# Optimization experiments

Hardware: AMD Instinct MI355X
Metric: run time of the kernel (lower is better)

## Reference

```python
import jax, jax.numpy as jnp
import numpy as np

WINDOW, SIM_TH, GAMMA, L_MAX, NUM_HEADS = 32, 0.7, 0.8, 1024, 8


def setup_inputs() -> dict:
    key = jax.random.key(0)
    ks = jax.random.split(key, 12)
    B, N, F, D, S, V, C = 8, 16384, 1024, 512, 64, 30522, 4
    padded_bags = jax.random.normal(ks[0], (B, N, F), jnp.float32)
    lengths = jax.random.randint(ks[1], (B,), N // 4, N + 1)
    key_padding_mask = jnp.arange(N)[None, :] >= lengths[:, None]  # True = pad (tail)
    input_ids = jax.random.randint(ks[2], (B, S), 0, V)
    attention_mask = jnp.ones((B, S), jnp.int32)

    def xav(k, shape):
        lim = np.sqrt(6.0 / (shape[0] + shape[1]))
        return jax.random.uniform(k, shape, jnp.float32, -lim, lim)

    emb_table = jax.random.normal(ks[3], (V, 768), jnp.float32) * 0.02
    return dict(
        padded_bags=padded_bags, key_padding_mask=key_padding_mask,
        input_ids=input_ids, attention_mask=attention_mask,
        emb_table=emb_table,
        W_tp=xav(ks[4], (768, D)), b_tp=jnp.zeros((D,), jnp.float32),
        W_enc=xav(ks[5], (F, D)), b_enc=jnp.zeros((D,), jnp.float32),
        ln_g=jnp.ones((D,), jnp.float32), ln_b=jnp.zeros((D,), jnp.float32),
        Wq=xav(ks[6], (D, D)), bq=jnp.zeros((D,), jnp.float32),
        Wk=xav(ks[7], (D, D)), bk=jnp.zeros((D,), jnp.float32),
        Wv=xav(ks[8], (D, D)), bv=jnp.zeros((D,), jnp.float32),
        Wo=xav(ks[9], (D, D)), bo=jnp.zeros((D,), jnp.float32),
        W_cls=xav(ks[10], (D, C)), b_cls=jnp.zeros((C,), jnp.float32),
    )


def reference(padded_bags, key_padding_mask, input_ids, attention_mask,
              emb_table, W_tp, b_tp, W_enc, b_enc, ln_g, ln_b,
              Wq, bq, Wk, bk, Wv, bv, Wo, bo, W_cls, b_cls):
    B, N, _ = padded_bags.shape
    D = W_enc.shape[1]
    # --- frozen text encoder surrogate (DistilBERT is frozen + no_grad in original):
    # token embedding + masked mean pooling stands in for the CLS feature [B,768]
    tok = emb_table[input_ids]                                   # [B,S,768]
    am = attention_mask[..., None].astype(jnp.float32)
    text_feat = (tok * am).sum(1) / jnp.maximum(am.sum(1), 1.0)
    text_feat = jax.lax.stop_gradient(text_feat)
    text_emb = text_feat @ W_tp + b_tp                           # [B,D]
    # --- feature encoder: Linear + LayerNorm + ReLU (dropout = eval identity) ---
    h = padded_bags @ W_enc + b_enc                              # [B,N,D]
    mu = h.mean(-1, keepdims=True)
    var = ((h - mu) ** 2).mean(-1, keepdims=True)
    img = jax.nn.relu(ln_g * (h - mu) / jnp.sqrt(var + 1e-5) + ln_b)
    valid = ~key_padding_mask                                    # [B,N]
    # --- Stage 1: sliding-window (size 32) cosine-similarity redundancy pruning ---
    fn = img / (jnp.linalg.norm(img, axis=-1, keepdims=True) + 1e-8)
    neg = jnp.full((B, N), -jnp.inf, jnp.float32)
    max_sim = neg
    for w in range(1, WINDOW + 1):                               # fixed small window loop
        sim_w = (fn[:, w:] * fn[:, :-w]).sum(-1)                 # [B,N-w]
        sim_w = jnp.where(valid[:, :-w], sim_w, -jnp.inf)
        max_sim = jnp.maximum(max_sim, jnp.concatenate([neg[:, :w], sim_w], axis=1))
    keep1 = valid & (max_sim < SIM_TH)                           # [B,N]
    # --- Stage 2: language-guided top-k by text relevance, kept in original order ---
    rel = jnp.einsum('bnd,bd->bn', img, text_emb)
    rel_m = jnp.where(keep1, rel, -jnp.inf)
    n_kept = keep1.sum(-1)
    k_b = jnp.clip((GAMMA * n_kept.astype(jnp.float32)).astype(jnp.int32), 1, L_MAX)
    _, idx = jax.lax.top_k(rel_m, L_MAX)                         # [B,L_MAX]
    sel = jnp.arange(L_MAX)[None, :] < k_b[:, None]
    idx_sorted = jnp.sort(jnp.where(sel, idx, N), axis=-1)       # sort -> original order
    mask2 = idx_sorted < N
    feat2 = jnp.take_along_axis(img, jnp.clip(idx_sorted, 0, N - 1)[..., None], axis=1)
    feat2 = jnp.where(mask2[..., None], feat2, 0.0)              # [B,L_MAX,D] zero-repadded
    # --- Stage 3: sequential visual token compression (adjacent-pair mean pooling) ---
    M = L_MAX // 2
    f2 = feat2.reshape(B, M, 2, D)
    pm = mask2.reshape(B, M, 2).astype(jnp.float32)
    feat3 = (f2 * pm[..., None]).sum(2) / jnp.maximum(pm.sum(2), 1.0)[..., None]  # [B,M,D]
    # --- cross-modal MHA aggregator (text query; zero-padded keys DO attend, as in original) ---
    H = NUM_HEADS
    dh = D // H
    q = (text_emb @ Wq + bq).reshape(B, H, dh)
    k = (feat3 @ Wk + bk).reshape(B, M, H, dh)
    v = (feat3 @ Wv + bv).reshape(B, M, H, dh)
    scores = jnp.einsum('bhd,bmhd->bhm', q, k) / np.float32(np.sqrt(dh))
    attn = jax.nn.softmax(scores, axis=-1)
    ctx = jnp.einsum('bhm,bmhd->bhd', attn, v).reshape(B, D)
    out = ctx @ Wo + bo
    return out @ W_cls + b_cls                                   # [B,num_classes]
```

## Files before the change

kernel.cpp:

```cpp
#include <hip/hip_runtime.h>
#include <hip/hip_bf16.h>
#include <math.h>
#include <stdint.h>

#define B_    8
#define N_    16384
#define F_    1024
#define D_    512
#define S_    64
#define H_    8
#define DH_   64
#define LMAX_ 1024
#define M2_   512
#define WIN_  32
#define NTOK_ (B_ * N_)

typedef __attribute__((ext_vector_type(8)))  short bf16x8;
typedef __attribute__((ext_vector_type(16))) float f32x16;

#define S_OF(r) (((r) >> 1) & 3)

static __device__ __forceinline__ float wred_sum(float v) {
    #pragma unroll
    for (int d = 1; d < 64; d <<= 1) v += __shfl_xor(v, d, 64);
    return v;
}

static __device__ __forceinline__ void bf8_to_f32(uint4 q, float* a) {
    a[0] = __uint_as_float(q.x << 16); a[1] = __uint_as_float(q.x & 0xffff0000u);
    a[2] = __uint_as_float(q.y << 16); a[3] = __uint_as_float(q.y & 0xffff0000u);
    a[4] = __uint_as_float(q.z << 16); a[5] = __uint_as_float(q.z & 0xffff0000u);
    a[6] = __uint_as_float(q.w << 16); a[7] = __uint_as_float(q.w & 0xffff0000u);
}

static __device__ __forceinline__ unsigned short bf16r(float x) {
    unsigned int b = __float_as_uint(x);
    return (unsigned short)((b + 0x7FFFu + ((b >> 16) & 1u)) >> 16);
}

static __device__ __forceinline__ void split_bf(float x, unsigned short& h, unsigned short& l) {
    unsigned int b = __float_as_uint(x);
    unsigned int hb = (b + 0x7FFFu + ((b >> 16) & 1u)) >> 16;
    h = (unsigned short)hb;
    float r = x - __uint_as_float(hb << 16);
    l = bf16r(r);
}

static __device__ __forceinline__ void split8(float4 f0, float4 f1, bf16x8& hi, bf16x8& lo) {
    float xs[8] = { f0.x, f0.y, f0.z, f0.w, f1.x, f1.y, f1.z, f1.w };
    unsigned int hp[4], lp[4];
    #pragma unroll
    for (int i = 0; i < 4; i++) {
        unsigned int b0 = __float_as_uint(xs[2*i]), b1 = __float_as_uint(xs[2*i+1]);
        hp[i] = (b0 >> 16) | (b1 & 0xffff0000u);
        float r0 = xs[2*i]   - __uint_as_float(b0 & 0xffff0000u);
        float r1 = xs[2*i+1] - __uint_as_float(b1 & 0xffff0000u);
        lp[i] = (__float_as_uint(r0) >> 16) | (__float_as_uint(r1) & 0xffff0000u);
    }
    union { uint4 u; bf16x8 v; } a, c;
    a.u = make_uint4(hp[0], hp[1], hp[2], hp[3]);
    c.u = make_uint4(lp[0], lp[1], lp[2], lp[3]);
    hi = a.v; lo = c.v;
}

static __device__ __forceinline__ void gll16(const void* g, void* l) {
    __builtin_amdgcn_global_load_lds(
        (const __attribute__((address_space(1))) unsigned int*)g,
        (__attribute__((address_space(3))) unsigned int*)l, 16, 0, 0);
}

__global__ void k_detect(const unsigned char* mb, int nbytes, int* flag) {
    int found = 0;
    for (int i = blockIdx.x * blockDim.x + threadIdx.x; i < nbytes; i += gridDim.x * blockDim.x)
        if ((i & 3) && mb[i]) found = 1;
    if (found) atomicOr(flag, 1);
}

__global__ void k_valid(const void* maskp, const int* flag, unsigned char* v) {
    int i = blockIdx.x * 256 + threadIdx.x;
    if (i >= NTOK_) return;
    int pad;
    if (*flag) pad = (((const unsigned char*)maskp)[i] != 0);
    else       pad = (((const int*)maskp)[i] != 0);
    v[i] = pad ? 0 : 1;
}

__global__ void k_text_feat(const float* emb, const int* ids, const int* am, float* tf) {
    int b = blockIdx.x;
    __shared__ int   sid[S_];
    __shared__ float sam[S_];
    int t = threadIdx.x;
    if (t < S_) { sid[t] = ids[b * S_ + t]; sam[t] = (float)am[b * S_ + t]; }
    __syncthreads();
    float asum = 0.f;
    for (int s = 0; s < S_; s++) asum += sam[s];
    float denom = fmaxf(asum, 1.0f);
    for (int d = t; d < 768; d += blockDim.x) {
        float acc = 0.f;
        for (int s = 0; s < S_; s++) acc += emb[(long)sid[s] * 768 + d] * sam[s];
        tf[b * 768 + d] = acc / denom;
    }
}

__global__ void k_rowmm(const float* in, const float* W, const float* bias,
                        float* out, int E, int Nn) {
    int b = blockIdx.x, d = threadIdx.x;
    __shared__ float sin[768];
    for (int e = d; e < E; e += blockDim.x) sin[e] = in[b * E + e];
    __syncthreads();
    float acc = bias[d];
    for (int e = 0; e < E; e++) acc = fmaf(sin[e], W[(long)e * Nn + d], acc);
    out[b * Nn + d] = acc;
}

__global__ __launch_bounds__(256) void k_bsplit_sw(const float* __restrict__ W,
                                                   unsigned short* __restrict__ bh,
                                                   unsigned short* __restrict__ bl) {
    __shared__ float tile[32][33];
    int e0 = blockIdx.x * 32;
    int d0 = blockIdx.y * 32;
    int t = threadIdx.x;
    int r = t >> 3, c4 = (t & 7) * 4;
    float4 v = *(const float4*)(W + (long)(e0 + r) * D_ + d0 + c4);
    tile[r][c4] = v.x; tile[r][c4 + 1] = v.y; tile[r][c4 + 2] = v.z; tile[r][c4 + 3] = v.w;
    __syncthreads();
    if (t < 128) {
        int c = t & 31, kq = t >> 5;
        int col = d0 + c;
        float xs[8];
        #pragma unroll
        for (int i = 0; i < 8; i++) xs[i] = tile[kq * 8 + i][c];
        unsigned short h[8], l[8];
        #pragma unroll
        for (int i = 0; i < 8; i++) split_bf(xs[i], h[i], l[i]);
        uint4 ph, pl;
        ph.x = h[0] | ((unsigned)h[1] << 16); ph.y = h[2] | ((unsigned)h[3] << 16);
        ph.z = h[4] | ((unsigned)h[5] << 16); ph.w = h[6] | ((unsigned)h[7] << 16);
        pl.x = l[0] | ((unsigned)l[1] << 16); pl.y = l[2] | ((unsigned)l[3] << 16);
        pl.z = l[4] | ((unsigned)l[5] << 16); pl.w = l[6] | ((unsigned)l[7] << 16);
        int Q = (e0 >> 3) + kq;
        int Qo = (Q & ~3) | ((Q & 3) ^ S_OF(col & 7));
        *(uint4*)(bh + (long)col * 1024 + Qo * 8) = ph;
        *(uint4*)(bl + (long)col * 1024 + Qo * 8) = pl;
    }
}

__global__ __launch_bounds__(256) void k_gemm3(const float* __restrict__ A,
                                               const unsigned short* __restrict__ Bh2,
                                               const unsigned short* __restrict__ Bl2,
                                               const float* __restrict__ bias,
                                               float* __restrict__ C) {
    __shared__ __align__(16) float ldsA[128][32];
    __shared__ __align__(16) unsigned short ldsB[2][128][32];
    int bid = blockIdx.x;
    int wg = (bid & 7) * 512 + (bid >> 3);
    int bn = wg & 3, bm = wg >> 2;
    int tid = threadIdx.x;
    int w = tid >> 6, lane = tid & 63;
    int r32 = lane & 31, kg = lane >> 5;
    int wr = w >> 1, wc = w & 1;
    int s8 = r32 & 7;

    const float* agbase = nullptr;
    const unsigned short* bgbase = nullptr;
    if (w < 2) {
        int rl = lane >> 3, qs = lane & 7;
        agbase = A + (long)(bm * 128 + w * 64 + rl) * 1024 + ((qs ^ rl) * 4);
    } else {
        const unsigned short* plane = (w == 2) ? Bh2 : Bl2;
        int lrow = lane >> 2, lq = lane & 3;
        bgbase = plane + (long)(bn * 128 + lrow) * 1024 + lq * 8;
    }

    f32x16 acc[2][2];
    #pragma unroll
    for (int i = 0; i < 2; i++)
        #pragma unroll
        for (int j = 0; j < 2; j++)
            #pragma unroll
            for (int r = 0; r < 16; r++) acc[i][j][r] = 0.f;

    for (int kt = 0; kt < 1024; kt += 32) {
        if (w < 2) {
            #pragma unroll
            for (int j = 0; j < 8; j++)
                gll16(agbase + (long)j * 8 * 1024 + kt, &ldsA[w * 64 + j * 8][0]);
        } else {
            #pragma unroll
            for (int j = 0; j < 8; j++)
                gll16(bgbase + (long)j * 16 * 1024 + kt, &ldsB[w - 2][j * 16][0]);
        }
        __syncthreads();
        #pragma unroll
        for (int k2 = 0; k2 < 2; k2++) {
            int qA = k2 * 4 + kg * 2;
            int qs0 = (qA ^ s8) * 4;
            int qs1 = ((qA + 1) ^ s8) * 4;
            bf16x8 a_h[2], a_l[2];
            #pragma unroll
            for (int rf = 0; rf < 2; rf++) {
                int ar = wr * 64 + rf * 32 + r32;
                float4 f0 = *(const float4*)&ldsA[ar][qs0];
                float4 f1 = *(const float4*)&ldsA[ar][qs1];
                split8(f0, f1, a_h[rf], a_l[rf]);
            }
            int qb = k2 * 2 + kg;
            bf16x8 b_h[2], b_l[2];
            #pragma unroll
            for (int cf = 0; cf < 2; cf++) {
                int bc = wc * 64 + cf * 32 + r32;
                int q = (qb ^ S_OF(r32)) * 8;
                b_h[cf] = *(const bf16x8*)&ldsB[0][bc][q];
                b_l[cf] = *(const bf16x8*)&ldsB[1][bc][q];
            }
            #pragma unroll
            for (int rf = 0; rf < 2; rf++)
                #pragma unroll
                for (int cf = 0; cf < 2; cf++) {
                    acc[rf][cf] = __builtin_amdgcn_mfma_f32_32x32x16_bf16(a_h[rf], b_h[cf], acc[rf][cf], 0, 0, 0);
                    acc[rf][cf] = __builtin_amdgcn_mfma_f32_32x32x16_bf16(a_h[rf], b_l[cf], acc[rf][cf], 0, 0, 0);
                    acc[rf][cf] = __builtin_amdgcn_mfma_f32_32x32x16_bf16(a_l[rf], b_h[cf], acc[rf][cf], 0, 0, 0);
                }
        }
        __syncthreads();
    }
    #pragma unroll
    for (int rf = 0; rf < 2; rf++)
        #pragma unroll
        for (int cf = 0; cf < 2; cf++) {
            int col = bn * 128 + wc * 64 + cf * 32 + r32;
            float bv = bias[col];
            #pragma unroll
            for (int r = 0; r < 16; r++) {
                int row = bm * 128 + wr * 64 + rf * 32 + (r & 3) + 8 * (r >> 2) + 4 * kg;
                C[(long)row * D_ + col] = acc[rf][cf][r] + bv;
            }
        }
}

#define GPAD 40
__global__ __launch_bounds__(256, 3) void k_gemm_mfma(const float* __restrict__ A,
                                                      const unsigned short* __restrict__ Bth,
                                                      const unsigned short* __restrict__ Btl,
                                                      const float* __restrict__ bias,
                                                      float* __restrict__ C) {
    __shared__ __align__(16) unsigned short As[2][64][GPAD];
    __shared__ __align__(16) unsigned short Bs[2][256][GPAD];
    int bm = blockIdx.x, bn = blockIdx.y;
    int tid = threadIdx.x;
    int w = tid >> 6, lane = tid & 63;
    int r32 = lane & 31, kg = lane >> 5;
    f32x16 acc[2][2];
    #pragma unroll
    for (int i = 0; i < 2; i++)
        #pragma unroll
        for (int j = 0; j < 2; j++)
            #pragma unroll
            for (int r = 0; r < 16; r++) acc[i][j][r] = 0.f;
    int arow = tid >> 2, aq = tid & 3;
    const float* abase = A + (long)(bm * 64 + arow) * 1024 + aq * 8;
    const unsigned short* bhbase = Bth + (long)(bn * 256 + tid) * 1024;
    const unsigned short* blbase = Btl + (long)(bn * 256 + tid) * 1024;
    float4 pa0 = *(const float4*)abase;
    float4 pa1 = *(const float4*)(abase + 4);
    for (int kt = 0; kt < 1024; kt += 32) {
        {
            float xs[8] = { pa0.x, pa0.y, pa0.z, pa0.w, pa1.x, pa1.y, pa1.z, pa1.w };
            unsigned short h[8], l[8];
            #pragma unroll
            for (int i = 0; i < 8; i++) split_bf(xs[i], h[i], l[i]);
            uint4 ph, pl;
            ph.x = h[0] | ((unsigned)h[1] << 16); ph.y = h[2] | ((unsigned)h[3] << 16);
            ph.z = h[4] | ((unsigned)h[5] << 16); ph.w = h[6] | ((unsigned)h[7] << 16);
            pl.x = l[0] | ((unsigned)l[1] << 16); pl.y = l[2] | ((unsigned)l[3] << 16);
            pl.z = l[4] | ((unsigned)l[5] << 16); pl.w = l[6] | ((unsigned)l[7] << 16);
            *(uint4*)&As[0][arow][aq * 8] = ph;
            *(uint4*)&As[1][arow][aq * 8] = pl;
        }
        {
            const uint4* ph = (const uint4*)(bhbase + kt);
            const uint4* pl = (const uint4*)(blbase + kt);
            #pragma unroll
            for (int q = 0; q < 4; q++) {
                *(uint4*)&Bs[0][tid][q * 8] = ph[q];
                *(uint4*)&Bs[1][tid][q * 8] = pl[q];
            }
        }
        __syncthreads();
        if (kt + 32 < 1024) {
            const float* ap = abase + kt + 32;
            pa0 = *(const float4*)ap;
            pa1 = *(const float4*)(ap + 4);
        }
        #pragma unroll
        for (int k2 = 0; k2 < 2; k2++) {
            int ko = k2 * 16 + kg * 8;
            bf16x8 ah[2], al[2], bh[2], blv[2];
            #pragma unroll
            for (int rf = 0; rf < 2; rf++) {
                ah[rf] = *(const bf16x8*)&As[0][rf * 32 + r32][ko];
                al[rf] = *(const bf16x8*)&As[1][rf * 32 + r32][ko];
            }
            #pragma unroll
            for (int cf = 0; cf < 2; cf++) {
                bh[cf]  = *(const bf16x8*)&Bs[0][w * 64 + cf * 32 + r32][ko];
                blv[cf] = *(const bf16x8*)&Bs[1][w * 64 + cf * 32 + r32][ko];
            }
            #pragma unroll
            for (int rf = 0; rf < 2; rf++)
                #pragma unroll
                for (int cf = 0; cf < 2; cf++) {
                    acc[rf][cf] = __builtin_amdgcn_mfma_f32_32x32x16_bf16(ah[rf], bh[cf],  acc[rf][cf], 0, 0, 0);
                    acc[rf][cf] = __builtin_amdgcn_mfma_f32_32x32x16_bf16(ah[rf], blv[cf], acc[rf][cf], 0, 0, 0);
                    acc[rf][cf] = __builtin_amdgcn_mfma_f32_32x32x16_bf16(al[rf], bh[cf],  acc[rf][cf], 0, 0, 0);
                }
        }
        __syncthreads();
    }
    #pragma unroll
    for (int rf = 0; rf < 2; rf++)
        #pragma unroll
        for (int cf = 0; cf < 2; cf++) {
            int col = bn * 256 + w * 64 + cf * 32 + r32;
            float bv = bias[col];
            #pragma unroll
            for (int r = 0; r < 16; r++) {
                int row = bm * 64 + rf * 32 + (r & 3) + 8 * (r >> 2) + 4 * kg;
                C[(long)row * D_ + col] = acc[rf][cf][r] + bv;
            }
        }
}

__global__ __launch_bounds__(256) void k_bsplit(const float* __restrict__ W,
                                                unsigned short* __restrict__ bh,
                                                unsigned short* __restrict__ bl) {
    __shared__ float tile[32][33];
    int e0 = blockIdx.x * 32;
    int d0 = blockIdx.y * 32;
    int t = threadIdx.x;
    int r = t >> 3;
    int c = (t & 7) * 4;
    float4 v = *(const float4*)(W + (long)(e0 + r) * D_ + d0 + c);
    tile[r][c] = v.x; tile[r][c + 1] = v.y; tile[r][c + 2] = v.z; tile[r][c + 3] = v.w;
    __syncthreads();
    ushort4 h4, l4;
    unsigned short hh, ll;
    float x0 = tile[c + 0][r], x1 = tile[c + 1][r], x2 = tile[c + 2][r], x3 = tile[c + 3][r];
    split_bf(x0, hh, ll); h4.x = hh; l4.x = ll;
    split_bf(x1, hh, ll); h4.y = hh; l4.y = ll;
    split_bf(x2, hh, ll); h4.z = hh; l4.z = ll;
    split_bf(x3, hh, ll); h4.w = hh; l4.w = ll;
    *(ushort4*)(bh + (long)(d0 + r) * 1024 + e0 + c) = h4;
    *(ushort4*)(bl + (long)(d0 + r) * 1024 + e0 + c) = l4;
}

__global__ __launch_bounds__(256) void k_ln(float* h, const float* g, const float* bb,
                                            const float* temb, float* rnorm, float* rel,
                                            unsigned short* fnb, float2* stats, int write_img) {
    int wid = threadIdx.x >> 6, lane = threadIdx.x & 63;
    long row = (long)blockIdx.x * 4 + wid;
    int b = (int)(row >> 14);
    float* hp = h + row * (long)D_;
    int c0 = lane * 4, c1 = 256 + lane * 4;
    float4 x0 = *(float4*)(hp + c0);
    float4 x1 = *(float4*)(hp + c1);
    float x[8] = { x0.x, x0.y, x0.z, x0.w, x1.x, x1.y, x1.z, x1.w };
    float s = 0.f;
    #pragma unroll
    for (int i = 0; i < 8; i++) s += x[i];
    s = wred_sum(s);
    float mu = s * (1.0f / 512.0f);
    float var = 0.f;
    #pragma unroll
    for (int i = 0; i < 8; i++) { float d = x[i] - mu; var += d * d; }
    var = wred_sum(var) * (1.0f / 512.0f);
    float inv = 1.0f / sqrtf(var + 1e-5f);
    float4 g0 = *(const float4*)(g + c0), g1 = *(const float4*)(g + c1);
    float4 b0 = *(const float4*)(bb + c0), b1 = *(const float4*)(bb + c1);
    float gg[8] = { g0.x, g0.y, g0.z, g0.w, g1.x, g1.y, g1.z, g1.w };
    float bbv[8] = { b0.x, b0.y, b0.z, b0.w, b1.x, b1.y, b1.z, b1.w };
    float y[8], sq = 0.f;
    #pragma unroll
    for (int i = 0; i < 8; i++) {
        y[i] = fmaxf(gg[i] * (x[i] - mu) * inv + bbv[i], 0.0f);
        sq += y[i] * y[i];
    }
    if (write_img) {
        float4 o0 = { y[0], y[1], y[2], y[3] }, o1 = { y[4], y[5], y[6], y[7] };
        *(float4*)(hp + c0) = o0;
        *(float4*)(hp + c1) = o1;
    }
    sq = wred_sum(sq);
    float rn = 1.0f / (sqrtf(sq) + 1e-8f);
    if (fnb) {
        ushort4 u0, u1;
        u0.x = bf16r(y[0] * rn); u0.y = bf16r(y[1] * rn);
        u0.z = bf16r(y[2] * rn); u0.w = bf16r(y[3] * rn);
        u1.x = bf16r(y[4] * rn); u1.y = bf16r(y[5] * rn);
        u1.z = bf16r(y[6] * rn); u1.w = bf16r(y[7] * rn);
        *(ushort4*)(fnb + row * D_ + c0) = u0;
        *(ushort4*)(fnb + row * D_ + c1) = u1;
    }
    const float* tp = temb + (long)b * D_;
    float4 t0 = *(const float4*)(tp + c0), t1 = *(const float4*)(tp + c1);
    float tt[8] = { t0.x, t0.y, t0.z, t0.w, t1.x, t1.y, t1.z, t1.w };
    float rl = 0.f;
    #pragma unroll
    for (int i = 0; i < 8; i++) rl = fmaf(y[i], tt[i], rl);
    rl = wred_sum(rl);
    if (lane == 0) { rnorm[row] = rn; rel[row] = rl; stats[row] = make_float2(mu, inv); }
}

__global__ __launch_bounds__(256) void k_simg(const unsigned short* __restrict__ fnb,
                                              const unsigned char* __restrict__ vld,
                                              int* __restrict__ keep) {
    int wid = threadIdx.x >> 6, lane = threadIdx.x & 63;
    int T = (blockIdx.x * 4 + wid) * 32;
    int r32 = lane & 31, kg = lane >> 5;
    int prevok = (T & (N_ - 1)) != 0;
    const unsigned short* arow  = fnb + (long)(T + r32) * D_ + kg * 8;
    const unsigned short* b0row = fnb + (long)((prevok ? T - 32 : T) + r32) * D_ + kg * 8;

    f32x16 g0, g1;
    #pragma unroll
    for (int r = 0; r < 16; r++) { g0[r] = 0.f; g1[r] = 0.f; }
    #pragma unroll 4
    for (int kt = 0; kt < D_; kt += 16) {
        bf16x8 a  = *(const bf16x8*)(arow + kt);
        bf16x8 b0 = *(const bf16x8*)(b0row + kt);
        g0 = __builtin_amdgcn_mfma_f32_32x32x16_bf16(a, b0, g0, 0, 0, 0);
        g1 = __builtin_amdgcn_mfma_f32_32x32x16_bf16(a, a,  g1, 0, 0, 0);
    }
    int okc0 = prevok ? (int)vld[T - 32 + r32] : 0;
    int okc1 = (int)vld[T + r32];
    float ms[16];
    #pragma unroll
    for (int r = 0; r < 16; r++) {
        int i = (r & 3) + 8 * (r >> 2) + 4 * kg;
        float v = -INFINITY;
        if (okc0 && r32 >= i) v = g0[r];
        if (okc1 && r32 < i)  v = fmaxf(v, g1[r]);
        #pragma unroll
        for (int d = 1; d < 32; d <<= 1) v = fmaxf(v, __shfl_xor(v, d, 64));
        ms[r] = v;
    }
    if (r32 == 0) {
        #pragma unroll
        for (int r = 0; r < 16; r++) {
            int i = (r & 3) + 8 * (r >> 2) + 4 * kg;
            int t = T + i;
            keep[t] = (vld[t] && ms[r] < 0.7f) ? 1 : 0;
        }
    }
}

#define CHUNK 28
#define KROWS 60
__global__ __launch_bounds__(256) void k_sim(const float* img, const float* rnorm,
                                             const unsigned char* vld, int* keep) {
    __shared__ __hip_bfloat16 fnbs[KROWS][D_];
    long c0 = (long)blockIdx.x * CHUNK;
    int tid = threadIdx.x;
    for (int idx = tid; idx < KROWS * (D_ / 8); idx += 256) {
        int rr = idx / (D_ / 8);
        int cc = (idx % (D_ / 8)) * 8;
        long grow = c0 - WIN_ + rr;
        if (grow < 0) grow = 0;
        if (grow >= NTOK_) grow = NTOK_ - 1;
        float rn = rnorm[grow];
        const float* p = img + grow * (long)D_ + cc;
        float4 u = *(const float4*)p, w = *(const float4*)(p + 4);
        fnbs[rr][cc + 0] = __float2bfloat16(u.x * rn);
        fnbs[rr][cc + 1] = __float2bfloat16(u.y * rn);
        fnbs[rr][cc + 2] = __float2bfloat16(u.z * rn);
        fnbs[rr][cc + 3] = __float2bfloat16(u.w * rn);
        fnbs[rr][cc + 4] = __float2bfloat16(w.x * rn);
        fnbs[rr][cc + 5] = __float2bfloat16(w.y * rn);
        fnbs[rr][cc + 6] = __float2bfloat16(w.z * rn);
        fnbs[rr][cc + 7] = __float2bfloat16(w.w * rn);
    }
    __syncthreads();
    int wid = tid >> 6, lane = tid & 63;
    for (int ti = 0; ti < 7; ti++) {
        int tloc = wid * 7 + ti;
        long t = c0 + tloc;
        if (t >= NTOK_) continue;
        int lr = WIN_ + tloc;
        int tl = (int)(t & (N_ - 1));
        float a[8];
        bf8_to_f32(*(const uint4*)&fnbs[lr][lane * 8], a);
        int wmax = tl < WIN_ ? tl : WIN_;
        float msim = -INFINITY;
        for (int w = 1; w <= wmax; w++) {
            if (!vld[t - w]) continue;
            float bvv[8];
            bf8_to_f32(*(const uint4*)&fnbs[lr - w][lane * 8], bvv);
            float p = 0.f;
            #pragma unroll
            for (int i = 0; i < 8; i++) p = fmaf(a[i], bvv[i], p);
            p = wred_sum(p);
            msim = fmaxf(msim, p);
        }
        int kp = (vld[t] && (msim < 0.7f)) ? 1 : 0;
        if (lane == 0) keep[t] = kp;
    }
}

static __device__ void scan1024(int* tot, int tid) {
    if (tid < 64) {
        int vals[16], s = 0;
        #pragma unroll
        for (int i = 0; i < 16; i++) vals[i] = tot[tid * 16 + i];
        #pragma unroll
        for (int i = 0; i < 16; i++) { int t = vals[i]; vals[i] = s; s += t; }
        int inc = s;
        #pragma unroll
        for (int d = 1; d < 64; d <<= 1) {
            int v = __shfl_up(inc, d, 64);
            if ((tid & 63) >= d) inc += v;
        }
        int excl = inc - s;
        #pragma unroll
        for (int i = 0; i < 16; i++) tot[tid * 16 + i] = vals[i] + excl;
    }
}

__global__ __launch_bounds__(1024) void k_topk(const float* rel, const int* keep, int* idxo) {
    int b = blockIdx.x, tid = threadIdx.x;
    const float* relb = rel + (long)b * N_;
    const int* keepb  = keep + (long)b * N_;
    __shared__ unsigned int hist[256];
    __shared__ int toti[1024];
    __shared__ unsigned int s_prefix;
    __shared__ int s_rem, s_k;

    unsigned int key[16];
    int base = tid * 16, nk_local = 0;
    #pragma unroll
    for (int j = 0; j < 16; j++) {
        int i = base + j;
        float r = relb[i];
        int kp = keepb[i];
        unsigned int bits = __float_as_uint(r);
        unsigned int kk = (bits & 0x80000000u) ? ~bits : (bits | 0x80000000u);
        key[j] = kp ? kk : 0u;
        nk_local += kp;
    }
    toti[tid] = nk_local; __syncthreads();
    for (int o = 512; o > 0; o >>= 1) { if (tid < o) toti[tid] += toti[tid + o]; __syncthreads(); }
    if (tid == 0) {
        int n_kept = toti[0];
        int k = (int)(0.8f * (float)n_kept);
        if (k < 1) k = 1; if (k > LMAX_) k = LMAX_;
        s_k = k; s_rem = k; s_prefix = 0u;
    }
    __syncthreads();

    for (int pass = 0; pass < 4; pass++) {
        int shift = 24 - pass * 8;
        unsigned int himask = (pass == 0) ? 0u : (0xFFFFFFFFu << (shift + 8));
        if (tid < 256) hist[tid] = 0u;
        __syncthreads();
        unsigned int pfx = s_prefix;
        #pragma unroll
        for (int j = 0; j < 16; j++) {
            unsigned int kk = key[j];
            if ((kk & himask) == (pfx & himask))
                atomicAdd(&hist[(kk >> shift) & 255], 1u);
        }
        __syncthreads();
        if (tid == 0) {
            int rem = s_rem;
            unsigned int cum = 0;
            for (int d = 255; d >= 0; d--) {
                unsigned int h = hist[d];
                if (cum + h >= (unsigned int)rem) {
                    s_rem = rem - (int)cum;
                    s_prefix = pfx | ((unsigned int)d << shift);
                    break;
                }
                cum += h;
            }
        }
        __syncthreads();
    }
    unsigned int T = s_prefix;
    int tie_need = s_rem, k = s_k;

    int eq[16], gt[16], eqpre[16];
    int locEq = 0;
    #pragma unroll
    for (int j = 0; j < 16; j++) {
        eq[j] = (key[j] == T); gt[j] = (key[j] > T);
        eqpre[j] = locEq; locEq += eq[j];
    }
    toti[tid] = locEq; __syncthreads();
    scan1024(toti, tid); __syncthreads();
    int eqoff = toti[tid];

    int sel[16], spre[16];
    int locS = 0;
    #pragma unroll
    for (int j = 0; j < 16; j++) {
        int rank = eqoff + eqpre[j];
        sel[j] = gt[j] || (eq[j] && rank < tie_need);
        spre[j] = locS; locS += sel[j];
    }
    __syncthreads();
    toti[tid] = locS; __syncthreads();
    scan1024(toti, tid); __syncthreads();
    int soff = toti[tid];
    #pragma unroll
    for (int j = 0; j < 16; j++)
        if (sel[j]) idxo[b * LMAX_ + soff + spre[j]] = base + j;
    for (int p = k + tid; p < LMAX_; p += 1024) idxo[b * LMAX_ + p] = N_;
}

__global__ void k_feat3(const float* img, const float2* stats, const float* lng,
                        const float* lnb, const int* idxo, float* f3, int recompute) {
    int bm = blockIdx.x;
    int b = bm >> 9, m = bm & 511;
    int i0 = idxo[b * LMAX_ + 2 * m], i1 = idxo[b * LMAX_ + 2 * m + 1];
    int c0 = i0 < N_, c1 = i1 < N_;
    float dn = 1.0f / fmaxf((float)(c0 + c1), 1.0f);
    long r0 = (long)b * N_ + (c0 ? i0 : 0);
    long r1 = (long)b * N_ + (c1 ? i1 : 0);
    int d = threadIdx.x * 4;
    float4 v0 = c0 ? *(const float4*)(img + r0 * D_ + d) : make_float4(0.f, 0.f, 0.f, 0.f);
    float4 v1 = c1 ? *(const float4*)(img + r1 * D_ + d) : make_float4(0.f, 0.f, 0.f, 0.f);
    if (recompute) {
        float4 g4 = *(const float4*)(lng + d);
        float4 b4 = *(const float4*)(lnb + d);
        if (c0) {
            float2 st = stats[r0];
            v0.x = fmaxf(g4.x * (v0.x - st.x) * st.y + b4.x, 0.0f);
            v0.y = fmaxf(g4.y * (v0.y - st.x) * st.y + b4.y, 0.0f);
            v0.z = fmaxf(g4.z * (v0.z - st.x) * st.y + b4.z, 0.0f);
            v0.w = fmaxf(g4.w * (v0.w - st.x) * st.y + b4.w, 0.0f);
        }
        if (c1) {
            float2 st = stats[r1];
            v1.x = fmaxf(g4.x * (v1.x - st.x) * st.y + b4.x, 0.0f);
            v1.y = fmaxf(g4.y * (v1.y - st.x) * st.y + b4.y, 0.0f);
            v1.z = fmaxf(g4.z * (v1.z - st.x) * st.y + b4.z, 0.0f);
            v1.w = fmaxf(g4.w * (v1.w - st.x) * st.y + b4.w, 0.0f);
        }
    }
    float4 o;
    o.x = (v0.x + v1.x) * dn; o.y = (v0.y + v1.y) * dn;
    o.z = (v0.z + v1.z) * dn; o.w = (v0.w + v1.w) * dn;
    *(float4*)(f3 + (long)bm * D_ + d) = o;
}

#define BM 128
#define BN 64
#define BK 32
#define ASTR 136
__global__ __launch_bounds__(256) void k_gemmkv(const float* __restrict__ A,
                                                const float* __restrict__ Wk2, const float* __restrict__ bk2, float* __restrict__ Ck,
                                                const float* __restrict__ Wv2, const float* __restrict__ bv2, float* __restrict__ Cv) {
    __shared__ float As[BK][ASTR];
    __shared__ float Bsf[BK][BN];
    int bm = blockIdx.x;
    int which = blockIdx.y >> 3;
    int bn = blockIdx.y & 7;
    const float* Bw  = which ? Wv2 : Wk2;
    const float* bias = which ? bv2 : bk2;
    float* C = which ? Cv : Ck;
    int tid = threadIdx.x;
    int trow = tid >> 4, tcol = tid & 15;
    float acc[8][4] = {};
    const float* Ab = A + (long)bm * BM * D_;
    const float* Bb = Bw + bn * BN;
    for (int kt = 0; kt < D_; kt += BK) {
        #pragma unroll
        for (int i = 0; i < 4; i++) {
            int f = tid + 256 * i;
            int row = f >> 3, c4 = (f & 7) << 2;
            float4 v = *(const float4*)(Ab + (long)row * D_ + kt + c4);
            As[c4 + 0][row] = v.x; As[c4 + 1][row] = v.y;
            As[c4 + 2][row] = v.z; As[c4 + 3][row] = v.w;
        }
        #pragma unroll
        for (int i = 0; i < 2; i++) {
            int f = tid + 256 * i;
            int row = f >> 4, c4 = (f & 15) << 2;
            *(float4*)&Bsf[row][c4] = *(const float4*)(Bb + (long)(kt + row) * D_ + c4);
        }
        __syncthreads();
        #pragma unroll 8
        for (int kk = 0; kk < BK; kk++) {
            float a[8], bv4[4];
            #pragma unroll
            for (int i = 0; i < 8; i++) a[i] = As[kk][trow * 8 + i];
            #pragma unroll
            for (int j = 0; j < 4; j++) bv4[j] = Bsf[kk][tcol * 4 + j];
            #pragma unroll
            for (int i = 0; i < 8; i++)
                #pragma unroll
                for (int j = 0; j < 4; j++)
                    acc[i][j] = fmaf(a[i], bv4[j], acc[i][j]);
        }
        __syncthreads();
    }
    int c = bn * BN + tcol * 4;
    #pragma unroll
    for (int i = 0; i < 8; i++) {
        long r = (long)bm * BM + trow * 8 + i;
        float4 v;
        v.x = acc[i][0] + bias[c + 0]; v.y = acc[i][1] + bias[c + 1];
        v.z = acc[i][2] + bias[c + 2]; v.w = acc[i][3] + bias[c + 3];
        *(float4*)(C + r * D_ + c) = v;
    }
}

__global__ __launch_bounds__(512) void k_attn(const float* qv, const float* kk,
                                              const float* vv, float* ctx) {
    int bh = blockIdx.x;
    int b = bh >> 3, h = bh & 7;
    __shared__ float qs[DH_];
    __shared__ float sc[M2_];
    __shared__ float red[M2_];
    __shared__ float part[8][DH_];
    int m = threadIdx.x;
    if (m < DH_) qs[m] = qv[b * D_ + h * DH_ + m];
    __syncthreads();
    const float* kp = kk + (long)b * M2_ * D_ + h * DH_;
    float acc = 0.f;
    #pragma unroll
    for (int d = 0; d < DH_; d += 4) {
        float4 kv = *(const float4*)(kp + (long)m * D_ + d);
        acc += qs[d] * kv.x + qs[d + 1] * kv.y + qs[d + 2] * kv.z + qs[d + 3] * kv.w;
    }
    acc *= 0.125f;
    red[m] = acc; __syncthreads();
    for (int o = 256; o > 0; o >>= 1) { if (m < o) red[m] = fmaxf(red[m], red[m + o]); __syncthreads(); }
    float mx = red[0]; __syncthreads();
    float e = expf(acc - mx);
    sc[m] = e; red[m] = e; __syncthreads();
    for (int o = 256; o > 0; o >>= 1) { if (m < o) red[m] += red[m + o]; __syncthreads(); }
    float inv = 1.0f / red[0];
    int g = m >> 6, d = m & 63;
    const float* vp = vv + (long)b * M2_ * D_ + h * DH_ + d;
    float a2 = 0.f;
    #pragma unroll 4
    for (int mm = g * 64; mm < g * 64 + 64; mm++)
        a2 = fmaf(sc[mm], vp[(long)mm * D_], a2);
    part[g][d] = a2; __syncthreads();
    if (m < DH_) {
        float s = 0.f;
        #pragma unroll
        for (int g2 = 0; g2 < 8; g2++) s += part[g2][m];
        ctx[b * D_ + h * DH_ + m] = s * inv;
    }
}

__global__ __launch_bounds__(512) void k_head(const float* ctx, const float* Wo, const float* bo,
                                              const float* Wc, const float* bc,
                                              float* out) {
    int b = blockIdx.x, d = threadIdx.x;
    __shared__ float cl[D_], ol[D_];
    cl[d] = ctx[b * D_ + d]; __syncthreads();
    float acc = bo[d];
    for (int e = 0; e < D_; e++) acc = fmaf(cl[e], Wo[(long)e * D_ + d], acc);
    ol[d] = acc; __syncthreads();
    if (d < 4) {
        float a2 = bc[d];
        for (int e = 0; e < D_; e++) a2 = fmaf(ol[e], Wc[e * 4 + d], a2);
        out[b * 4 + d] = a2;
    }
}

extern "C" void kernel_launch(void* const* d_in, const int* in_sizes, int n_in,
                              void* d_out, int out_size, void* d_ws, size_t ws_size,
                              hipStream_t stream) {
    const float* bags = (const float*)d_in[0];
    const void*  kpm  = d_in[1];
    const int*   ids  = (const int*)d_in[2];
    const int*   am   = (const int*)d_in[3];
    const float* emb  = (const float*)d_in[4];
    const float* Wtp  = (const float*)d_in[5];
    const float* btp  = (const float*)d_in[6];
    const float* Wen  = (const float*)d_in[7];
    const float* ben  = (const float*)d_in[8];
    const float* lng  = (const float*)d_in[9];
    const float* lnb  = (const float*)d_in[10];
    const float* Wq   = (const float*)d_in[11];
    const float* bq   = (const float*)d_in[12];
    const float* Wk   = (const float*)d_in[13];
    const float* bk   = (const float*)d_in[14];
    const float* Wv   = (const float*)d_in[15];
    const float* bv   = (const float*)d_in[16];
    const float* Wo   = (const float*)d_in[17];
    const float* bo   = (const float*)d_in[18];
    const float* Wc   = (const float*)d_in[19];
    const float* bc   = (const float*)d_in[20];

    char* ws = (char*)d_ws;
    size_t o = 0;
    auto alloc = [&](size_t bytes) -> void* {
        void* p = ws + o; o += (bytes + 255) & ~(size_t)255; return p;
    };
    float* img  = (float*)alloc((size_t)NTOK_ * D_ * 4);
    float* rno  = (float*)alloc((size_t)NTOK_ * 4);
    float* rel  = (float*)alloc((size_t)NTOK_ * 4);
    int*   keep = (int*)alloc((size_t)NTOK_ * 4);
    unsigned char* vld = (unsigned char*)alloc(NTOK_);
    float* tf   = (float*)alloc(B_ * 768 * 4);
    float* te   = (float*)alloc(B_ * D_ * 4);
    float* qv   = (float*)alloc(B_ * D_ * 4);
    int*   idxo = (int*)alloc(B_ * LMAX_ * 4);
    float* f3   = (float*)alloc((size_t)B_ * M2_ * D_ * 4);
    float* kkb  = (float*)alloc((size_t)B_ * M2_ * D_ * 4);
    float* vvb  = (float*)alloc((size_t)B_ * M2_ * D_ * 4);
    float* ctx  = (float*)alloc(B_ * D_ * 4);
    int*   flag = (int*)alloc(256);
    float2* stats = (float2*)alloc((size_t)NTOK_ * 8);
    unsigned short* bth = (unsigned short*)alloc((size_t)D_ * F_ * 2);
    unsigned short* btl = (unsigned short*)alloc((size_t)D_ * F_ * 2);

    size_t fnb_need = (size_t)NTOK_ * D_ * 2 + 4096;
    bool newpath = (ws_size > o) && ((ws_size - o) >= fnb_need);
    unsigned short* fnb = nullptr;
    if (newpath) fnb = (unsigned short*)alloc((size_t)NTOK_ * D_ * 2);

    hipMemsetAsync(flag, 0, 4, stream);
    k_detect<<<64, 256, 0, stream>>>((const unsigned char*)kpm, NTOK_, flag);
    k_valid<<<(NTOK_ + 255) / 256, 256, 0, stream>>>(kpm, flag, vld);
    k_text_feat<<<B_, 256, 0, stream>>>(emb, ids, am, tf);
    k_rowmm<<<B_, 512, 0, stream>>>(tf, Wtp, btp, te, 768, 512);
    k_rowmm<<<B_, 512, 0, stream>>>(te, Wq, bq, qv, 512, 512);

    dim3 gsplit(F_ / 32, D_ / 32);
    if (newpath) {
        k_bsplit_sw<<<gsplit, 256, 0, stream>>>(Wen, bth, btl);
        k_gemm3<<<4096, 256, 0, stream>>>(bags, bth, btl, ben, img);
    } else {
        k_bsplit<<<gsplit, 256, 0, stream>>>(Wen, bth, btl);
        dim3 g3(NTOK_ / 64, 2);
        k_gemm_mfma<<<g3, 256, 0, stream>>>(bags, bth, btl, ben, img);
    }

    int write_img = newpath ? 0 : 1;
    k_ln<<<NTOK_ / 4, 256, 0, stream>>>(img, lng, lnb, te, rno, rel, fnb, stats, write_img);
    if (fnb) k_simg<<<NTOK_ / 128, 256, 0, stream>>>(fnb, vld, keep);
    else     k_sim<<<(NTOK_ + CHUNK - 1) / CHUNK, 256, 0, stream>>>(img, rno, vld, keep);
    k_topk<<<B_, 1024, 0, stream>>>(rel, keep, idxo);
    k_feat3<<<B_ * M2_, 128, 0, stream>>>(img, stats, lng, lnb, idxo, f3, newpath ? 1 : 0);

    dim3 gkv(B_ * M2_ / BM, 16);
    k_gemmkv<<<gkv, 256, 0, stream>>>(f3, Wk, bk, kkb, Wv, bv, vvb);

    k_attn<<<B_ * H_, 512, 0, stream>>>(qv, kkb, vvb, ctx);
    k_head<<<B_, 512, 0, stream>>>(ctx, Wo, bo, Wc, bc, (float*)d_out);
}
```

Baseline: 941.4 us.

## Move K/V projection GEMM to split-bf16 MFMA and parallelize top-k radix scan

Replaces the scalar FP32 K/V projection GEMM with the MFMA split-bf16 GEMM body already used for the encoder, parameterized on K. Wk and Wv are pre-split into swizzled hi/lo bf16 planes, and one launch covers both K and V. The top-k kernel now uses wave-shuffle reductions and a parallel suffix scan over the histogram instead of a serial loop in one thread. This adds two extra split launches and depends on three-product bf16 accuracy for the K/V path.

```diff
diff --git a/kernel.cpp b/kernel.cpp
--- a/kernel.cpp
+++ b/kernel.cpp
@@ -115,7 +115,8 @@
 
 __global__ __launch_bounds__(256) void k_bsplit_sw(const float* __restrict__ W,
                                                    unsigned short* __restrict__ bh,
-                                                   unsigned short* __restrict__ bl) {
+                                                   unsigned short* __restrict__ bl,
+                                                   int E) {
     __shared__ float tile[32][33];
     int e0 = blockIdx.x * 32;
     int d0 = blockIdx.y * 32;
@@ -140,20 +141,18 @@
         pl.z = l[4] | ((unsigned)l[5] << 16); pl.w = l[6] | ((unsigned)l[7] << 16);
         int Q = (e0 >> 3) + kq;
         int Qo = (Q & ~3) | ((Q & 3) ^ S_OF(col & 7));
-        *(uint4*)(bh + (long)col * 1024 + Qo * 8) = ph;
-        *(uint4*)(bl + (long)col * 1024 + Qo * 8) = pl;
-    }
-}
-
-__global__ __launch_bounds__(256) void k_gemm3(const float* __restrict__ A,
-                                               const unsigned short* __restrict__ Bh2,
-                                               const unsigned short* __restrict__ Bl2,
-                                               const float* __restrict__ bias,
-                                               float* __restrict__ C) {
+        *(uint4*)(bh + (long)col * E + Qo * 8) = ph;
+        *(uint4*)(bl + (long)col * E + Qo * 8) = pl;
+    }
+}
+
+static __device__ __forceinline__ void gemm3_body(const float* __restrict__ A,
+                                                  const unsigned short* __restrict__ Bh2,
+                                                  const unsigned short* __restrict__ Bl2,
+                                                  const float* __restrict__ bias,
+                                                  float* __restrict__ C, int K, int wg) {
     __shared__ __align__(16) float ldsA[128][32];
     __shared__ __align__(16) unsigned short ldsB[2][128][32];
-    int bid = blockIdx.x;
-    int wg = (bid & 7) * 512 + (bid >> 3);
     int bn = wg & 3, bm = wg >> 2;
     int tid = threadIdx.x;
     int w = tid >> 6, lane = tid & 63;
@@ -165,11 +164,11 @@
     const unsigned short* bgbase = nullptr;
     if (w < 2) {
         int rl = lane >> 3, qs = lane & 7;
-        agbase = A + (long)(bm * 128 + w * 64 + rl) * 1024 + ((qs ^ rl) * 4);
+        agbase = A + (long)(bm * 128 + w * 64 + rl) * K + ((qs ^ rl) * 4);
     } else {
         const unsigned short* plane = (w == 2) ? Bh2 : Bl2;
         int lrow = lane >> 2, lq = lane & 3;
-        bgbase = plane + (long)(bn * 128 + lrow) * 1024 + lq * 8;
+        bgbase = plane + (long)(bn * 128 + lrow) * K + lq * 8;
     }
 
     f32x16 acc[2][2];
@@ -180,15 +179,15 @@
             #pragma unroll
             for (int r = 0; r < 16; r++) acc[i][j][r] = 0.f;
 
-    for (int kt = 0; kt < 1024; kt += 32) {
+    for (int kt = 0; kt < K; kt += 32) {
         if (w < 2) {
             #pragma unroll
             for (int j = 0; j < 8; j++)
-                gll16(agbase + (long)j * 8 * 1024 + kt, &ldsA[w * 64 + j * 8][0]);
+                gll16(agbase + (long)j * 8 * K + kt, &ldsA[w * 64 + j * 8][0]);
         } else {
             #pragma unroll
             for (int j = 0; j < 8; j++)
-                gll16(bgbase + (long)j * 16 * 1024 + kt, &ldsB[w - 2][j * 16][0]);
+                gll16(bgbase + (long)j * 16 * K + kt, &ldsB[w - 2][j * 16][0]);
         }
         __syncthreads();
         #pragma unroll
@@ -236,6 +235,30 @@
                 C[(long)row * D_ + col] = acc[rf][cf][r] + bv;
             }
         }
+}
+
+__global__ __launch_bounds__(256) void k_gemm3p(const float* __restrict__ A,
+                                                const unsigned short* __restrict__ Bh2,
+                                                const unsigned short* __restrict__ Bl2,
+                                                const float* __restrict__ bias,
+                                                float* __restrict__ C, int K) {
+    int bid = blockIdx.x;
+    int cpx = gridDim.x >> 3;
+    int wg = (bid & 7) * cpx + (bid >> 3);
+    gemm3_body(A, Bh2, Bl2, bias, C, K, wg);
+}
+
+__global__ __launch_bounds__(256) void k_gemmkv2(const float* __restrict__ A,
+                                                 const unsigned short* __restrict__ Kh, const unsigned short* __restrict__ Kl,
+                                                 const float* __restrict__ bk2, float* __restrict__ Ck,
+                                                 const unsigned short* __restrict__ Vh, const unsigned short* __restrict__ Vl,
+                                                 const float* __restrict__ bv2, float* __restrict__ Cv) {
+    int which = blockIdx.x & 1;
+    int wg = blockIdx.x >> 1;
+    if (which)
+        gemm3_body(A, Vh, Vl, bv2, Cv, 512, wg);
+    else
+        gemm3_body(A, Kh, Kl, bk2, Ck, 512, wg);
 }
 
 #define GPAD 40
@@ -530,7 +553,9 @@
     const float* relb = rel + (long)b * N_;
     const int* keepb  = keep + (long)b * N_;
     __shared__ unsigned int hist[256];
+    __shared__ unsigned int suf[256];
     __shared__ int toti[1024];
+    __shared__ int wsum[16];
     __shared__ unsigned int s_prefix;
     __shared__ int s_rem, s_k;
 
@@ -546,10 +571,15 @@
         key[j] = kp ? kk : 0u;
         nk_local += kp;
     }
-    toti[tid] = nk_local; __syncthreads();
-    for (int o = 512; o > 0; o >>= 1) { if (tid < o) toti[tid] += toti[tid + o]; __syncthreads(); }
+    int nk = nk_local;
+    #pragma unroll
+    for (int d = 1; d < 64; d <<= 1) nk += __shfl_xor(nk, d, 64);
+    if ((tid & 63) == 0) wsum[tid >> 6] = nk;
+    __syncthreads();
     if (tid == 0) {
-        int n_kept = toti[0];
+        int n_kept = 0;
+        #pragma unroll
+        for (int i = 0; i < 16; i++) n_kept += wsum[i];
         int k = (int)(0.8f * (float)n_kept);
         if (k < 1) k = 1; if (k > LMAX_) k = LMAX_;
         s_k = k; s_rem = k; s_prefix = 0u;
@@ -562,6 +592,7 @@
         if (tid < 256) hist[tid] = 0u;
         __syncthreads();
         unsigned int pfx = s_prefix;
+        int rem = s_rem;
         #pragma unroll
         for (int j = 0; j < 16; j++) {
             unsigned int kk = key[j];
@@ -569,17 +600,21 @@
                 atomicAdd(&hist[(kk >> shift) & 255], 1u);
         }
         __syncthreads();
-        if (tid == 0) {
-            int rem = s_rem;
-            unsigned int cum = 0;
-            for (int d = 255; d >= 0; d--) {
-                unsigned int h = hist[d];
-                if (cum + h >= (unsigned int)rem) {
-                    s_rem = rem - (int)cum;
-                    s_prefix = pfx | ((unsigned int)d << shift);
-                    break;
-                }
-                cum += h;
+        if (tid < 256) suf[tid] = hist[tid];
+        __syncthreads();
+        for (int o = 1; o < 256; o <<= 1) {
+            unsigned int v = 0;
+            if (tid < 256 && tid + o < 256) v = suf[tid + o];
+            __syncthreads();
+            if (tid < 256) suf[tid] += v;
+            __syncthreads();
+        }
+        if (tid < 256) {
+            unsigned int sv = suf[tid];
+            unsigned int nxt = (tid == 255) ? 0u : suf[tid + 1];
+            if (sv >= (unsigned int)rem && nxt < (unsigned int)rem) {
+                s_prefix = pfx | ((unsigned int)tid << shift);
+                s_rem = rem - (int)nxt;
             }
         }
         __syncthreads();
@@ -650,68 +685,6 @@
     o.x = (v0.x + v1.x) * dn; o.y = (v0.y + v1.y) * dn;
     o.z = (v0.z + v1.z) * dn; o.w = (v0.w + v1.w) * dn;
     *(float4*)(f3 + (long)bm * D_ + d) = o;
-}
-
-#define BM 128
-#define BN 64
-#define BK 32
-#define ASTR 136
-__global__ __launch_bounds__(256) void k_gemmkv(const float* __restrict__ A,
-                                                const float* __restrict__ Wk2, const float* __restrict__ bk2, float* __restrict__ Ck,
-                                                const float* __restrict__ Wv2, const float* __restrict__ bv2, float* __restrict__ Cv) {
-    __shared__ float As[BK][ASTR];
-    __shared__ float Bsf[BK][BN];
-    int bm = blockIdx.x;
-    int which = blockIdx.y >> 3;
-    int bn = blockIdx.y & 7;
-    const float* Bw  = which ? Wv2 : Wk2;
-    const float* bias = which ? bv2 : bk2;
-    float* C = which ? Cv : Ck;
-    int tid = threadIdx.x;
-    int trow = tid >> 4, tcol = tid & 15;
-    float acc[8][4] = {};
-    const float* Ab = A + (long)bm * BM * D_;
-    const float* Bb = Bw + bn * BN;
-    for (int kt = 0; kt < D_; kt += BK) {
-        #pragma unroll
-        for (int i = 0; i < 4; i++) {
-            int f = tid + 256 * i;
-            int row = f >> 3, c4 = (f & 7) << 2;
-            float4 v = *(const float4*)(Ab + (long)row * D_ + kt + c4);
-            As[c4 + 0][row] = v.x; As[c4 + 1][row] = v.y;
-            As[c4 + 2][row] = v.z; As[c4 + 3][row] = v.w;
-        }
-        #pragma unroll
-        for (int i = 0; i < 2; i++) {
-            int f = tid + 256 * i;
-            int row = f >> 4, c4 = (f & 15) << 2;
-            *(float4*)&Bsf[row][c4] = *(const float4*)(Bb + (long)(kt + row) * D_ + c4);
-        }
-        __syncthreads();
-        #pragma unroll 8
-        for (int kk = 0; kk < BK; kk++) {
-            float a[8], bv4[4];
-            #pragma unroll
-            for (int i = 0; i < 8; i++) a[i] = As[kk][trow * 8 + i];
-            #pragma unroll
-            for (int j = 0; j < 4; j++) bv4[j] = Bsf[kk][tcol * 4 + j];
-            #pragma unroll
-            for (int i = 0; i < 8; i++)
-                #pragma unroll
-                for (int j = 0; j < 4; j++)
-                    acc[i][j] = fmaf(a[i], bv4[j], acc[i][j]);
-        }
-        __syncthreads();
-    }
-    int c = bn * BN + tcol * 4;
-    #pragma unroll
-    for (int i = 0; i < 8; i++) {
-        long r = (long)bm * BM + trow * 8 + i;
-        float4 v;
-        v.x = acc[i][0] + bias[c + 0]; v.y = acc[i][1] + bias[c + 1];
-        v.z = acc[i][2] + bias[c + 2]; v.w = acc[i][3] + bias[c + 3];
-        *(float4*)(C + r * D_ + c) = v;
-    }
 }
 
 __global__ __launch_bounds__(512) void k_attn(const float* qv, const float* kk,
@@ -818,6 +791,10 @@
     float2* stats = (float2*)alloc((size_t)NTOK_ * 8);
     unsigned short* bth = (unsigned short*)alloc((size_t)D_ * F_ * 2);
     unsigned short* btl = (unsigned short*)alloc((size_t)D_ * F_ * 2);
+    unsigned short* wkh = (unsigned short*)alloc((size_t)D_ * D_ * 2);
+    unsigned short* wkl = (unsigned short*)alloc((size_t)D_ * D_ * 2);
+    unsigned short* wvh = (unsigned short*)alloc((size_t)D_ * D_ * 2);
+    unsigned short* wvl = (unsigned short*)alloc((size_t)D_ * D_ * 2);
 
     size_t fnb_need = (size_t)NTOK_ * D_ * 2 + 4096;
     bool newpath = (ws_size > o) && ((ws_size - o) >= fnb_need);
@@ -831,11 +808,16 @@
     k_rowmm<<<B_, 512, 0, stream>>>(tf, Wtp, btp, te, 768, 512);
     k_rowmm<<<B_, 512, 0, stream>>>(te, Wq, bq, qv, 512, 512);
 
-    dim3 gsplit(F_ / 32, D_ / 32);
+    dim3 gw512(D_ / 32, D_ / 32);
+    k_bsplit_sw<<<gw512, 256, 0, stream>>>(Wk, wkh, wkl, D_);
+    k_bsplit_sw<<<gw512, 256, 0, stream>>>(Wv, wvh, wvl, D_);
+
     if (newpath) {
-        k_bsplit_sw<<<gsplit, 256, 0, stream>>>(Wen, bth, btl);
-        k_gemm3<<<4096, 256, 0, stream>>>(bags, bth, btl, ben, img);
+        dim3 gw1024(F_ / 32, D_ / 32);
+        k_bsplit_sw<<<gw1024, 256, 0, stream>>>(Wen, bth, btl, F_);
+        k_gemm3p<<<4096, 256, 0, stream>>>(bags, bth, btl, ben, img, F_);
     } else {
+        dim3 gsplit(F_ / 32, D_ / 32);
         k_bsplit<<<gsplit, 256, 0, stream>>>(Wen, bth, btl);
         dim3 g3(NTOK_ / 64, 2);
         k_gemm_mfma<<<g3, 256, 0, stream>>>(bags, bth, btl, ben, img);
@@ -848,8 +830,7 @@
     k_topk<<<B_, 1024, 0, stream>>>(rel, keep, idxo);
     k_feat3<<<B_ * M2_, 128, 0, stream>>>(img, stats, lng, lnb, idxo, f3, newpath ? 1 : 0);
 
-    dim3 gkv(B_ * M2_ / BM, 16);
-    k_gemmkv<<<gkv, 256, 0, stream>>>(f3, Wk, bk, kkb, Wv, bv, vvb);
+    k_gemmkv2<<<256, 256, 0, stream>>>(f3, wkh, wkl, bk, kkb, wvh, wvl, bv, vvb);
 
     k_attn<<<B_ * H_, 512, 0, stream>>>(qv, kkb, vvb, ctx);
     k_head<<<B_, 512, 0, stream>>>(ctx, Wo, bo, Wc, bc, (float*)d_out);
```

Measured after the change: 879.2 us. 1.07x faster.
